# Performance work log

Hardware: AMD Instinct MI355X
Metric: run time of the kernel (lower is better)

The kernel has to match this reference:

```python
import jax, jax.numpy as jnp
import numpy as np

HIDDEN_DIM = 2048
NUM_HEADS = 16
HEAD_DIM = HIDDEN_DIM // NUM_HEADS
BATCH = 2
SEQ = 2048


def setup_inputs() -> dict:
    key = jax.random.key(0)
    ks = jax.random.split(key, 5)
    scale = 1.0 / np.sqrt(HIDDEN_DIM)
    x = jax.random.normal(ks[0], (BATCH, SEQ, HIDDEN_DIM), dtype=jnp.float32)
    w_q = jax.random.normal(ks[1], (HIDDEN_DIM, HIDDEN_DIM), dtype=jnp.float32) * scale
    w_k = jax.random.normal(ks[2], (HIDDEN_DIM, HIDDEN_DIM), dtype=jnp.float32) * scale
    w_v = jax.random.normal(ks[3], (HIDDEN_DIM, HIDDEN_DIM), dtype=jnp.float32) * scale
    w_o = jax.random.normal(ks[4], (HIDDEN_DIM, HIDDEN_DIM), dtype=jnp.float32) * scale
    return {"x": x, "w_q": w_q, "w_k": w_k, "w_v": w_v, "w_o": w_o}


def reference(x, w_q, w_k, w_v, w_o):
    # Projections: x @ W.T  (weights stored as (out, in) like torch)
    q = jnp.einsum('bsd,ed->bse', x, w_q)
    k = jnp.einsum('bsd,ed->bse', x, w_k)
    v = jnp.einsum('bsd,ed->bse', x, w_v)
    b, s, _ = q.shape
    # split heads: (b, h, s, hd)
    q = q.reshape(b, s, NUM_HEADS, HEAD_DIM).transpose(0, 2, 1, 3)
    k = k.reshape(b, s, NUM_HEADS, HEAD_DIM).transpose(0, 2, 1, 3)
    v = v.reshape(b, s, NUM_HEADS, HEAD_DIM).transpose(0, 2, 1, 3)
    scale = 1.0 / np.sqrt(HEAD_DIM)
    # Online-softmax tiling in the source (causal=False default) is
    # mathematically identical to standard softmax attention.
    scores = jnp.einsum('bhqd,bhkd->bhqk', q, k) * scale
    p = jax.nn.softmax(scores, axis=-1)
    o = jnp.einsum('bhqk,bhkd->bhqd', p, v)
    o = o.transpose(0, 2, 1, 3).reshape(b, s, HIDDEN_DIM)
    return jnp.einsum('bsd,ed->bse', o, w_o)
```

## Files before the change

### kernel.cpp

```cpp
#include <hip/hip_runtime.h>


typedef _Float16 half8 __attribute__((ext_vector_type(8)));
typedef _Float16 half4 __attribute__((ext_vector_type(4)));
typedef float floatx4 __attribute__((ext_vector_type(4)));

__device__ __forceinline__ void async16(const void* g, void* l) {
  __builtin_amdgcn_global_load_lds((__attribute__((address_space(1))) void*)(g),
                                   (__attribute__((address_space(3))) void*)(l),
                                   16, 0, 0);
}

__global__ void cvt_all(const float* __restrict__ x, const float* __restrict__ w0,
                        const float* __restrict__ w1, const float* __restrict__ w2,
                        const float* __restrict__ w3, _Float16* __restrict__ xh,
                        _Float16* __restrict__ wh, float scale0) {
  int i = blockIdx.x * blockDim.x + threadIdx.x;
  const int XQ = 1 << 21;
  float sc = 1.0f;
  const float* src;
  _Float16* dst;
  int j;
  if (i < XQ) { src = x; dst = xh; j = i; }
  else {
    int t = i - XQ;
    int m = t >> 20;
    src = (m == 0) ? w0 : (m == 1) ? w1 : (m == 2) ? w2 : w3;
    if (m == 0) sc = scale0;
    dst = wh; j = t;
  }
  int js = (i < XQ) ? j : (j & ((1 << 20) - 1));
  float4 v = reinterpret_cast<const float4*>(src)[js];
  union { _Float16 h[4]; short4 s; } u;
  u.h[0] = (_Float16)(v.x * sc); u.h[1] = (_Float16)(v.y * sc);
  u.h[2] = (_Float16)(v.z * sc); u.h[3] = (_Float16)(v.w * sc);
  reinterpret_cast<short4*>(dst)[j] = u.s;
}

template <int OUT_MODE>
__global__ __launch_bounds__(256)
void gemm_nt(const _Float16* __restrict__ A, const _Float16* __restrict__ Bw,
             void* __restrict__ Cv, void* __restrict__ Cv2) {
  __shared__ _Float16 As[128 * 64];
  __shared__ _Float16 Bs[128 * 64];
  const int tid = threadIdx.x;
  const int wave = tid >> 6, lane = tid & 63;
  const int wm = wave >> 1, wn = wave & 1;
  const int l15 = lane & 15, l4 = lane >> 4;
  const int bm = blockIdx.y, bn = blockIdx.x;

  floatx4 acc[4][4] = {};

  for (int k0 = 0; k0 < 2048; k0 += 64) {
    __syncthreads();
#pragma unroll
    for (int i = 0; i < 4; ++i) {
      int c = i * 256 + tid;
      int row = c >> 3, cc = c & 7;
      int g = cc ^ (row & 7);
      async16(A + (size_t)(bm * 128 + row) * 2048 + k0 + g * 8, &As[c * 8]);
      async16(Bw + (size_t)(bn * 128 + row) * 2048 + k0 + g * 8, &Bs[c * 8]);
    }
    __syncthreads();
#pragma unroll
    for (int ks = 0; ks < 2; ++ks) {
      half8 af[4], bf[4];
      int ch = (ks * 4 + l4) ^ (l15 & 7);
#pragma unroll
      for (int t = 0; t < 4; ++t) {
        af[t] = *reinterpret_cast<const half8*>(&As[(wm * 64 + t * 16 + l15) * 64 + ch * 8]);
        bf[t] = *reinterpret_cast<const half8*>(&Bs[(wn * 64 + t * 16 + l15) * 64 + ch * 8]);
      }
#pragma unroll
      for (int mt = 0; mt < 4; ++mt)
#pragma unroll
        for (int nt = 0; nt < 4; ++nt)
          acc[mt][nt] = __builtin_amdgcn_mfma_f32_16x16x32_f16(af[mt], bf[nt], acc[mt][nt], 0, 0, 0);
    }
  }

  const int rbase = bm * 128 + wm * 64;
  const int cbase = bn * 128 + wn * 64;
  if constexpr (OUT_MODE == 0) {
    if (cbase < 4096) {
      _Float16* C = (_Float16*)Cv + (size_t)(cbase >> 11) * (4096ull * 2048);
#pragma unroll
      for (int mt = 0; mt < 4; ++mt)
#pragma unroll
        for (int nt = 0; nt < 4; ++nt) {
          int r0 = rbase + mt * 16 + l4 * 4;
          int cg = (cbase + nt * 16 + l15) & 2047;
#pragma unroll
          for (int r = 0; r < 4; ++r)
            C[(size_t)(r0 + r) * 2048 + cg] = (_Float16)acc[mt][nt][r];
        }
    } else {
      _Float16* C = (_Float16*)Cv2;
#pragma unroll
      for (int mt = 0; mt < 4; ++mt)
#pragma unroll
        for (int nt = 0; nt < 4; ++nt) {
          int m0 = rbase + mt * 16 + l4 * 4;
          int d = cbase + nt * 16 + l15 - 4096;
          size_t base = (size_t)(m0 >> 11) * (2048ull * 2048) + (size_t)d * 2048 + (m0 & 2047);
          union { _Float16 h[4]; short4 s; } u;
#pragma unroll
          for (int r = 0; r < 4; ++r) u.h[r] = (_Float16)acc[mt][nt][r];
          *reinterpret_cast<short4*>(C + base) = u.s;
        }
    }
  } else {
    float* C = (float*)Cv;
#pragma unroll
    for (int mt = 0; mt < 4; ++mt)
#pragma unroll
      for (int nt = 0; nt < 4; ++nt) {
        int r0 = rbase + mt * 16 + l4 * 4;
        int cg = cbase + nt * 16 + l15;
#pragma unroll
        for (int r = 0; r < 4; ++r)
          C[(size_t)(r0 + r) * 2048 + cg] = acc[mt][nt][r];
      }
  }
}

__global__ __launch_bounds__(256, 2)
void flash_attn(const _Float16* __restrict__ Q, const _Float16* __restrict__ Kg,
                const _Float16* __restrict__ Vt, _Float16* __restrict__ O) {
  __shared__ _Float16 Ks[64 * 128];
  __shared__ _Float16 Vs[128 * 64];
  __shared__ _Float16 Ps[128 * 64];
  const int tid = threadIdx.x, wave = tid >> 6, lane = tid & 63;
  const int l15 = lane & 15, l4 = lane >> 4;
  const int bh = blockIdx.y, b = bh >> 4, h = bh & 15;
  const int q0 = blockIdx.x * 128;

  const _Float16* Qp = Q + ((size_t)(b * 2048 + q0 + wave * 32)) * 2048 + h * 128;
  const _Float16* Kp = Kg + (size_t)b * 2048 * 2048 + h * 128;
  const _Float16* Vp = Vt + (size_t)b * 2048 * 2048 + (size_t)(h * 128) * 2048;

  half8 qf[2][4];
#pragma unroll
  for (int qt = 0; qt < 2; ++qt)
#pragma unroll
    for (int ks = 0; ks < 4; ++ks)
      qf[qt][ks] = *reinterpret_cast<const half8*>(
          Qp + (size_t)(qt * 16 + l15) * 2048 + ks * 32 + l4 * 8);

  floatx4 oacc[2][8] = {};
  float lsumq[2] = {0.f, 0.f};

  for (int k0 = 0; k0 < 2048; k0 += 64) {
    __syncthreads();
#pragma unroll
    for (int i = 0; i < 4; ++i) {
      int c = i * 256 + tid;
      int row = c >> 4, cc = c & 15;
      int g = cc ^ (row & 15);
      async16(Kp + (size_t)(k0 + row) * 2048 + g * 8, &Ks[c * 8]);
    }
#pragma unroll
    for (int i = 0; i < 4; ++i) {
      int c = i * 256 + tid;
      int row = c >> 3, cc = c & 7;
      int g = cc ^ (row & 7);
      async16(Vp + (size_t)row * 2048 + k0 + g * 8, &Vs[c * 8]);
    }
    __syncthreads();

    floatx4 sacc[4][2] = {};
#pragma unroll
    for (int ks = 0; ks < 4; ++ks) {
      half8 kf[4];
#pragma unroll
      for (int st = 0; st < 4; ++st) {
        int row = st * 16 + l15;
        int ch = (ks * 4 + l4) ^ l15;
        kf[st] = *reinterpret_cast<const half8*>(&Ks[row * 128 + ch * 8]);
      }
#pragma unroll
      for (int st = 0; st < 4; ++st)
#pragma unroll
        for (int qt = 0; qt < 2; ++qt)
          sacc[st][qt] = __builtin_amdgcn_mfma_f32_16x16x32_f16(kf[st], qf[qt][ks], sacc[st][qt], 0, 0, 0);
    }

#pragma unroll
    for (int qt = 0; qt < 2; ++qt)
#pragma unroll
      for (int st = 0; st < 4; ++st) {
        float p0 = exp2f(sacc[st][qt][0]);
        float p1 = exp2f(sacc[st][qt][1]);
        float p2 = exp2f(sacc[st][qt][2]);
        float p3 = exp2f(sacc[st][qt][3]);
        lsumq[qt] += (p0 + p1) + (p2 + p3);
        half4 pv;
        pv[0] = (_Float16)p0; pv[1] = (_Float16)p1;
        pv[2] = (_Float16)p2; pv[3] = (_Float16)p3;
        int ch = (st * 2 + (l4 >> 1)) ^ (l15 & 7);
        *reinterpret_cast<half4*>(
            &Ps[(wave * 32 + qt * 16 + l15) * 64 + ch * 8 + (l4 & 1) * 4]) = pv;
      }

    __builtin_amdgcn_s_waitcnt(0xC07F);

#pragma unroll
    for (int ks2 = 0; ks2 < 2; ++ks2) {
      half8 pf[2];
#pragma unroll
      for (int mt = 0; mt < 2; ++mt)
        pf[mt] = *reinterpret_cast<const half8*>(
            &Ps[(wave * 32 + mt * 16 + l15) * 64 + (((ks2 * 4 + l4) ^ (l15 & 7)) * 8)]);
#pragma unroll
      for (int nt2 = 0; nt2 < 8; ++nt2) {
        int row = nt2 * 16 + l15;
        int ch = (ks2 * 4 + l4) ^ (row & 7);
        half8 vf = *reinterpret_cast<const half8*>(&Vs[row * 64 + ch * 8]);
#pragma unroll
        for (int mt = 0; mt < 2; ++mt)
          oacc[mt][nt2] = __builtin_amdgcn_mfma_f32_16x16x32_f16(pf[mt], vf, oacc[mt][nt2], 0, 0, 0);
      }
    }
  }

#pragma unroll
  for (int qt = 0; qt < 2; ++qt) {
    lsumq[qt] += __shfl_xor(lsumq[qt], 16);
    lsumq[qt] += __shfl_xor(lsumq[qt], 32);
  }

  _Float16* Op = O + ((size_t)(b * 2048 + q0 + wave * 32)) * 2048 + h * 128;
#pragma unroll
  for (int mt = 0; mt < 2; ++mt)
#pragma unroll
    for (int r = 0; r < 4; ++r) {
      float inv = 1.0f / __shfl(lsumq[mt], l4 * 4 + r);
#pragma unroll
      for (int nt2 = 0; nt2 < 8; ++nt2) {
        int row = mt * 16 + l4 * 4 + r;
        int col = nt2 * 16 + l15;
        Op[(size_t)row * 2048 + col] = (_Float16)(oacc[mt][nt2][r] * inv);
      }
    }
}

extern "C" void kernel_launch(void* const* d_in, const int* in_sizes, int n_in,
                              void* d_out, int out_size, void* d_ws, size_t ws_size,
                              hipStream_t stream) {
  const float* x = (const float*)d_in[0];
  const float* wq = (const float*)d_in[1];
  const float* wk = (const float*)d_in[2];
  const float* wv = (const float*)d_in[3];
  const float* wo = (const float*)d_in[4];
  float* out = (float*)d_out;

  const size_t XN = (size_t)4096 * 2048;
  const size_t WN = (size_t)2048 * 2048;
  _Float16* xh = (_Float16*)d_ws;
  _Float16* qh = xh + XN;
  _Float16* vth = xh + 3 * XN;
  _Float16* oh = xh + 4 * XN;
  _Float16* wqh = xh + 5 * XN;

  const float SM_SCALE = 0.08838834764831845f * 1.4426950408889634f;

  cvt_all<<<dim3(24576), 256, 0, stream>>>(x, wq, wk, wv, wo, xh, wqh, SM_SCALE);
  gemm_nt<0><<<dim3(48, 32), 256, 0, stream>>>(xh, wqh, qh, vth);
  flash_attn<<<dim3(16, 32), 256, 0, stream>>>(qh, qh + XN, vth, oh);
  gemm_nt<2><<<dim3(16, 32), 256, 0, stream>>>(oh, wqh + 3 * WN, out, nullptr);
}
```

Measured before the change: 392.2 us.

## Rewrite GEMM as 256x128 double-buffered ping-pong pipeline with 512 threads

Restructures the projection GEMM kernel to use 256x128 tiles with 8 waves, double-buffered LDS, and an interleaved schedule that issues async global-to-LDS loads between MFMA clusters guarded by fine-grained vmcnt waits and barriers. Adds s_setprio around MFMA groups and a swizzled block-to-tile mapping for L2 locality. Intended to hide global load latency behind compute and raise MFMA utilization, at the cost of more LDS per block and fragile manual waitcnt ordering.

```diff
diff --git a/kernel.cpp b/kernel.cpp
--- a/kernel.cpp
+++ b/kernel.cpp
@@ -37,59 +37,134 @@
   reinterpret_cast<short4*>(dst)[j] = u.s;
 }
 
+template <int MO, int NO>
+__device__ __forceinline__ void mmg(floatx4 (&acc)[4][4], const half8 (&af)[2][2],
+                                    const half8 (&bf)[2][2]) {
+#pragma unroll
+  for (int mt = 0; mt < 2; ++mt)
+#pragma unroll
+    for (int nt = 0; nt < 2; ++nt)
+#pragma unroll
+      for (int ks = 0; ks < 2; ++ks)
+        acc[MO + mt][NO + nt] = __builtin_amdgcn_mfma_f32_16x16x32_f16(
+            af[mt][ks], bf[nt][ks], acc[MO + mt][NO + nt], 0, 0, 0);
+}
+
+__device__ __forceinline__ void rdfrag(half8 (&f)[2][2], const _Float16* base,
+                                       int r0, int r1, int ch0, int ch1) {
+  f[0][0] = *reinterpret_cast<const half8*>(base + r0 * 64 + ch0);
+  f[0][1] = *reinterpret_cast<const half8*>(base + r0 * 64 + ch1);
+  f[1][0] = *reinterpret_cast<const half8*>(base + r1 * 64 + ch0);
+  f[1][1] = *reinterpret_cast<const half8*>(base + r1 * 64 + ch1);
+}
+
 template <int OUT_MODE>
-__global__ __launch_bounds__(256)
+__global__ __launch_bounds__(512, 2)
 void gemm_nt(const _Float16* __restrict__ A, const _Float16* __restrict__ Bw,
              void* __restrict__ Cv, void* __restrict__ Cv2) {
-  __shared__ _Float16 As[128 * 64];
-  __shared__ _Float16 Bs[128 * 64];
+  __shared__ _Float16 As[2][256 * 64];
+  __shared__ _Float16 Bs[2][128 * 64];
   const int tid = threadIdx.x;
   const int wave = tid >> 6, lane = tid & 63;
   const int wm = wave >> 1, wn = wave & 1;
   const int l15 = lane & 15, l4 = lane >> 4;
-  const int bm = blockIdx.y, bn = blockIdx.x;
+
+  const int nwg = gridDim.x << 4;
+  const int orig = blockIdx.x * 16 + blockIdx.y;
+  const int swz = (orig & 7) * (nwg >> 3) + (orig >> 3);
+  const int bm = swz & 15, bn = swz >> 4;
+
+  const _Float16* ag[4]; int al[4];
+#pragma unroll
+  for (int j = 0; j < 4; ++j) {
+    int c = j * 512 + tid, row = c >> 3, g = (c & 7) ^ (row & 7);
+    ag[j] = A + (size_t)(bm * 256 + row) * 2048 + g * 8;
+    al[j] = c * 8;
+  }
+  const _Float16* bg[2]; int bl[2];
+#pragma unroll
+  for (int j = 0; j < 2; ++j) {
+    int c = j * 512 + tid, row = c >> 3, g = (c & 7) ^ (row & 7);
+    bg[j] = Bw + (size_t)(bn * 128 + row) * 2048 + g * 8;
+    bl[j] = c * 8;
+  }
+
+  const int rm = wm * 16 + l15;
+  const int rn = wn * 16 + l15;
+  const int ch0 = (l4 ^ (l15 & 7)) * 8;
+  const int ch1 = ((l4 + 4) ^ (l15 & 7)) * 8;
+
+#pragma unroll
+  for (int j = 0; j < 4; ++j) async16(ag[j], &As[0][al[j]]);
+#pragma unroll
+  for (int j = 0; j < 2; ++j) async16(bg[j], &Bs[0][bl[j]]);
+  asm volatile("s_waitcnt vmcnt(0)" ::: "memory");
+  __builtin_amdgcn_s_barrier();
 
   floatx4 acc[4][4] = {};
-
-  for (int k0 = 0; k0 < 2048; k0 += 64) {
-    __syncthreads();
-#pragma unroll
-    for (int i = 0; i < 4; ++i) {
-      int c = i * 256 + tid;
-      int row = c >> 3, cc = c & 7;
-      int g = cc ^ (row & 7);
-      async16(A + (size_t)(bm * 128 + row) * 2048 + k0 + g * 8, &As[c * 8]);
-      async16(Bw + (size_t)(bn * 128 + row) * 2048 + k0 + g * 8, &Bs[c * 8]);
-    }
-    __syncthreads();
-#pragma unroll
-    for (int ks = 0; ks < 2; ++ks) {
-      half8 af[4], bf[4];
-      int ch = (ks * 4 + l4) ^ (l15 & 7);
-#pragma unroll
-      for (int t = 0; t < 4; ++t) {
-        af[t] = *reinterpret_cast<const half8*>(&As[(wm * 64 + t * 16 + l15) * 64 + ch * 8]);
-        bf[t] = *reinterpret_cast<const half8*>(&Bs[(wn * 64 + t * 16 + l15) * 64 + ch * 8]);
-      }
+  half8 afA[2][2], afB[2][2], bfA[2][2], bfB[2][2];
+
+#pragma unroll 2
+  for (int t = 0; t < 32; ++t) {
+    const _Float16* Ac = &As[t & 1][0];
+    const _Float16* Bc = &Bs[t & 1][0];
+    _Float16* An = &As[(t & 1) ^ 1][0];
+    _Float16* Bn = &Bs[(t & 1) ^ 1][0];
+    const int kn = t * 64 + 64;
+    const bool st = (t < 31);
+
+    asm volatile("s_waitcnt vmcnt(3)" ::: "memory");
+    rdfrag(afA, Ac, rm, rm + 64, ch0, ch1);
+    if (st) { async16(ag[0] + kn, An + al[0]); async16(ag[1] + kn, An + al[1]); }
+    __builtin_amdgcn_s_barrier();
+    __builtin_amdgcn_s_waitcnt(0xC07F);
+    __builtin_amdgcn_s_setprio(1);
+    if (t) mmg<2, 2>(acc, afB, bfB);
+    __builtin_amdgcn_s_setprio(0);
+    __builtin_amdgcn_s_barrier();
+
+    asm volatile("s_waitcnt vmcnt(4)" ::: "memory");
+    rdfrag(bfA, Bc, rn, rn + 32, ch0, ch1);
+    if (st) async16(bg[0] + kn, Bn + bl[0]);
+    __builtin_amdgcn_s_barrier();
+    __builtin_amdgcn_s_waitcnt(0xC07F);
+    __builtin_amdgcn_s_setprio(1);
+    mmg<0, 0>(acc, afA, bfA);
+    __builtin_amdgcn_s_setprio(0);
+    __builtin_amdgcn_s_barrier();
+
+    asm volatile("s_waitcnt vmcnt(3)" ::: "memory");
+    rdfrag(bfB, Bc, rn + 64, rn + 96, ch0, ch1);
+    if (st) async16(bg[1] + kn, Bn + bl[1]);
+    __builtin_amdgcn_s_barrier();
+    __builtin_amdgcn_s_waitcnt(0xC07F);
+    __builtin_amdgcn_s_setprio(1);
+    mmg<0, 2>(acc, afA, bfB);
+    __builtin_amdgcn_s_setprio(0);
+    __builtin_amdgcn_s_barrier();
+
+    asm volatile("s_waitcnt vmcnt(2)" ::: "memory");
+    rdfrag(afB, Ac, rm + 128, rm + 192, ch0, ch1);
+    if (st) { async16(ag[2] + kn, An + al[2]); async16(ag[3] + kn, An + al[3]); }
+    __builtin_amdgcn_s_barrier();
+    __builtin_amdgcn_s_waitcnt(0xC07F);
+    __builtin_amdgcn_s_setprio(1);
+    mmg<2, 0>(acc, afB, bfA);
+    __builtin_amdgcn_s_setprio(0);
+    __builtin_amdgcn_s_barrier();
+  }
+  mmg<2, 2>(acc, afB, bfB);
+
+  const int cb = bn * 128;
+  if constexpr (OUT_MODE == 0) {
+    if (cb < 4096) {
+      _Float16* C = (_Float16*)Cv + (size_t)(cb >> 11) * (4096ull * 2048);
 #pragma unroll
       for (int mt = 0; mt < 4; ++mt)
 #pragma unroll
-        for (int nt = 0; nt < 4; ++nt)
-          acc[mt][nt] = __builtin_amdgcn_mfma_f32_16x16x32_f16(af[mt], bf[nt], acc[mt][nt], 0, 0, 0);
-    }
-  }
-
-  const int rbase = bm * 128 + wm * 64;
-  const int cbase = bn * 128 + wn * 64;
-  if constexpr (OUT_MODE == 0) {
-    if (cbase < 4096) {
-      _Float16* C = (_Float16*)Cv + (size_t)(cbase >> 11) * (4096ull * 2048);
-#pragma unroll
-      for (int mt = 0; mt < 4; ++mt)
-#pragma unroll
         for (int nt = 0; nt < 4; ++nt) {
-          int r0 = rbase + mt * 16 + l4 * 4;
-          int cg = (cbase + nt * 16 + l15) & 2047;
+          int r0 = bm * 256 + mt * 64 + wm * 16 + l4 * 4;
+          int cg = (cb + nt * 32 + wn * 16 + l15) & 2047;
 #pragma unroll
           for (int r = 0; r < 4; ++r)
             C[(size_t)(r0 + r) * 2048 + cg] = (_Float16)acc[mt][nt][r];
@@ -100,8 +175,8 @@
       for (int mt = 0; mt < 4; ++mt)
 #pragma unroll
         for (int nt = 0; nt < 4; ++nt) {
-          int m0 = rbase + mt * 16 + l4 * 4;
-          int d = cbase + nt * 16 + l15 - 4096;
+          int m0 = bm * 256 + mt * 64 + wm * 16 + l4 * 4;
+          int d = cb + nt * 32 + wn * 16 + l15 - 4096;
           size_t base = (size_t)(m0 >> 11) * (2048ull * 2048) + (size_t)d * 2048 + (m0 & 2047);
           union { _Float16 h[4]; short4 s; } u;
 #pragma unroll
@@ -115,8 +190,8 @@
     for (int mt = 0; mt < 4; ++mt)
 #pragma unroll
       for (int nt = 0; nt < 4; ++nt) {
-        int r0 = rbase + mt * 16 + l4 * 4;
-        int cg = cbase + nt * 16 + l15;
+        int r0 = bm * 256 + mt * 64 + wm * 16 + l4 * 4;
+        int cg = cb + nt * 32 + wn * 16 + l15;
 #pragma unroll
         for (int r = 0; r < 4; ++r)
           C[(size_t)(r0 + r) * 2048 + cg] = acc[mt][nt][r];
@@ -265,7 +340,7 @@
   const float SM_SCALE = 0.08838834764831845f * 1.4426950408889634f;
 
   cvt_all<<<dim3(24576), 256, 0, stream>>>(x, wq, wk, wv, wo, xh, wqh, SM_SCALE);
-  gemm_nt<0><<<dim3(48, 32), 256, 0, stream>>>(xh, wqh, qh, vth);
+  gemm_nt<0><<<dim3(48, 16), 512, 0, stream>>>(xh, wqh, qh, vth);
   flash_attn<<<dim3(16, 32), 256, 0, stream>>>(qh, qh + XN, vth, oh);
-  gemm_nt<2><<<dim3(16, 32), 256, 0, stream>>>(oh, wqh + 3 * WN, out, nullptr);
-}
+  gemm_nt<2><<<dim3(16, 16), 512, 0, stream>>>(oh, wqh + 3 * WN, out, nullptr);
+}
```

After: 409.1 us. +4.3%, slower.

## Rewrite QKV projection GEMM as 256x256 double-buffered pipelined kernel

Applied to the files above, without the earlier changes.

Replaces the fused QKV projection GEMM with a 512-thread, 256x256-tile kernel. It double-buffers LDS, splits each k-step into four MFMA phases interleaved with async global-to-LDS loads and register-level fragment prefetch, and raises wave priority around MFMA bursts. It also swizzles the workgroup order for L2 locality. The aim is to hide load latency and raise MFMA utilisation in the largest GEMM, at the cost of 128KB of LDS, heavy register pressure and hand-tuned waitcnt counts that must stay correct. The output projection moves to a separate copy of the old kernel.

```diff
diff --git a/kernel.cpp b/kernel.cpp
--- a/kernel.cpp
+++ b/kernel.cpp
@@ -37,10 +37,180 @@
   reinterpret_cast<short4*>(dst)[j] = u.s;
 }
 
-template <int OUT_MODE>
-__global__ __launch_bounds__(256)
+__device__ __forceinline__ void rdA4(half8 (&f)[4][2], const _Float16* base,
+                                     int ch0, int ch1) {
+#pragma unroll
+  for (int mt = 0; mt < 4; ++mt) {
+    f[mt][0] = *reinterpret_cast<const half8*>(base + mt * 2048 + ch0);
+    f[mt][1] = *reinterpret_cast<const half8*>(base + mt * 2048 + ch1);
+  }
+}
+__device__ __forceinline__ void rdB2(half8 (&f)[2][2], const _Float16* base,
+                                     int ch0, int ch1) {
+#pragma unroll
+  for (int nt = 0; nt < 2; ++nt) {
+    f[nt][0] = *reinterpret_cast<const half8*>(base + nt * 4096 + ch0);
+    f[nt][1] = *reinterpret_cast<const half8*>(base + nt * 4096 + ch1);
+  }
+}
+template <int MO, int NO>
+__device__ __forceinline__ void mmg16(floatx4 (&acc)[8][4], const half8 (&af)[4][2],
+                                      const half8 (&bf)[2][2]) {
+#pragma unroll
+  for (int kk = 0; kk < 2; ++kk)
+#pragma unroll
+    for (int mt = 0; mt < 4; ++mt)
+#pragma unroll
+      for (int nt = 0; nt < 2; ++nt)
+        acc[MO + mt][NO + nt] = __builtin_amdgcn_mfma_f32_16x16x32_f16(
+            af[mt][kk], bf[nt][kk], acc[MO + mt][NO + nt], 0, 0, 0);
+}
+
+#define STAGE_AH0(buf, kk) { async16(ags + (kk), &(buf)[ldst]); \
+                             async16(ags + 131072 + (kk), &(buf)[4096 + ldst]); }
+#define STAGE_AH1(buf, kk) { async16(ags + 262144 + (kk), &(buf)[8192 + ldst]); \
+                             async16(ags + 393216 + (kk), &(buf)[12288 + ldst]); }
+#define STAGE_BH0(buf, kk) { async16(bgs + (kk), &(buf)[ldst]); \
+                             async16(bgs + 131072 + (kk), &(buf)[4096 + ldst]); }
+#define STAGE_BH1(buf, kk) { async16(bgs + 262144 + (kk), &(buf)[8192 + ldst]); \
+                             async16(bgs + 393216 + (kk), &(buf)[12288 + ldst]); }
+#define VMW(n) asm volatile("s_waitcnt vmcnt(" #n ")" ::: "memory")
+#define SBAR() __builtin_amdgcn_s_barrier()
+#define SCHED() __builtin_amdgcn_sched_barrier(0)
+#define PRIO1() __builtin_amdgcn_s_setprio(1)
+#define PRIO0() __builtin_amdgcn_s_setprio(0)
+
+__global__ __launch_bounds__(512, 2)
 void gemm_nt(const _Float16* __restrict__ A, const _Float16* __restrict__ Bw,
              void* __restrict__ Cv, void* __restrict__ Cv2) {
+  __shared__ _Float16 As[2][256 * 64];
+  __shared__ _Float16 Bs[2][256 * 64];
+  const int tid = threadIdx.x;
+  const int wave = tid >> 6, lane = tid & 63;
+  const int wm = wave >> 2, wn = wave & 3;
+  const int l15 = lane & 15, l4 = lane >> 4;
+
+  const int NBN = 24;
+  const int nwg = NBN * 16;
+  const int swz = (blockIdx.x & 7) * (nwg >> 3) + (blockIdx.x >> 3);
+  const int bn = swz % NBN, bm = swz / NBN;
+
+  const int srow = tid >> 3;
+  const int g = (tid & 7) ^ (srow & 7);
+  const _Float16* ags = A + (size_t)(bm * 256 + srow) * 2048 + g * 8;
+  const _Float16* bgs = Bw + (size_t)(bn * 256 + srow) * 2048 + g * 8;
+  const int ldst = tid * 8;
+
+  const int arow = wm * 16 + l15;
+  const int brow = wn * 16 + l15;
+  const int ch0 = (l4 ^ (l15 & 7)) * 8;
+  const int ch1 = ((l4 + 4) ^ (l15 & 7)) * 8;
+
+  STAGE_AH0(As[0], 0); STAGE_BH0(Bs[0], 0);
+  STAGE_BH1(Bs[0], 0); STAGE_AH1(As[0], 0);
+  STAGE_AH0(As[1], 64); STAGE_BH0(Bs[1], 64);
+  VMW(4);
+  SBAR();
+
+  floatx4 acc[8][4] = {};
+  half8 afA[4][2], afB[4][2], bfA[2][2], bfB[2][2];
+  rdA4(afA, &As[0][arow * 64], ch0, ch1);
+  rdB2(bfA, &Bs[0][brow * 64], ch0, ch1);
+
+#pragma unroll 2
+  for (int t = 0; t < 30; ++t) {
+    const int c = t & 1, nx = c ^ 1;
+    const int k1 = t * 64 + 64, k2 = t * 64 + 128;
+    const _Float16* Ac = &As[c][0];
+    const _Float16* Bc = &Bs[c][0];
+
+    PRIO1(); mmg16<0, 0>(acc, afA, bfA); PRIO0();
+    rdB2(bfB, Bc + brow * 64 + 8192, ch0, ch1);
+    STAGE_BH1(Bs[nx], k1);
+    SCHED(); VMW(6); SBAR();
+
+    PRIO1(); mmg16<0, 2>(acc, afA, bfB); PRIO0();
+    rdA4(afB, Ac + arow * 64 + 8192, ch0, ch1);
+    STAGE_AH1(As[nx], k1);
+    SCHED(); VMW(6); SBAR();
+
+    PRIO1(); mmg16<4, 0>(acc, afB, bfA); PRIO0();
+    STAGE_AH0(As[c], k2);
+    SCHED(); VMW(6); SBAR();
+
+    PRIO1(); mmg16<4, 2>(acc, afB, bfB); PRIO0();
+    rdA4(afA, &As[nx][arow * 64], ch0, ch1);
+    rdB2(bfA, &Bs[nx][brow * 64], ch0, ch1);
+    STAGE_BH0(Bs[c], k2);
+    SCHED(); VMW(6); SBAR();
+  }
+
+  {
+    const _Float16* Ac = &As[0][0];
+    const _Float16* Bc = &Bs[0][0];
+    PRIO1(); mmg16<0, 0>(acc, afA, bfA); PRIO0();
+    rdB2(bfB, Bc + brow * 64 + 8192, ch0, ch1);
+    STAGE_BH1(Bs[1], 1984);
+    SCHED(); VMW(6); SBAR();
+
+    PRIO1(); mmg16<0, 2>(acc, afA, bfB); PRIO0();
+    rdA4(afB, Ac + arow * 64 + 8192, ch0, ch1);
+    STAGE_AH1(As[1], 1984);
+    SCHED(); VMW(6); SBAR();
+
+    PRIO1(); mmg16<4, 0>(acc, afB, bfA); PRIO0();
+    SCHED(); VMW(4); SBAR();
+
+    PRIO1(); mmg16<4, 2>(acc, afB, bfB); PRIO0();
+    rdA4(afA, &As[1][arow * 64], ch0, ch1);
+    rdB2(bfA, &Bs[1][brow * 64], ch0, ch1);
+    SCHED(); VMW(2); SBAR();
+  }
+  {
+    const _Float16* Ac = &As[1][0];
+    const _Float16* Bc = &Bs[1][0];
+    PRIO1(); mmg16<0, 0>(acc, afA, bfA); PRIO0();
+    rdB2(bfB, Bc + brow * 64 + 8192, ch0, ch1);
+    SCHED(); VMW(0); SBAR();
+    PRIO1(); mmg16<0, 2>(acc, afA, bfB); PRIO0();
+    rdA4(afB, Ac + arow * 64 + 8192, ch0, ch1);
+    mmg16<4, 0>(acc, afB, bfA);
+    mmg16<4, 2>(acc, afB, bfB);
+  }
+
+  const int cb0 = bn * 256;
+  if (cb0 < 4096) {
+    _Float16* C = (_Float16*)Cv + (size_t)(cb0 >> 11) * (4096ull * 2048);
+#pragma unroll
+    for (int mt = 0; mt < 8; ++mt)
+#pragma unroll
+      for (int nt = 0; nt < 4; ++nt) {
+        int r0 = bm * 256 + mt * 32 + wm * 16 + l4 * 4;
+        int cg = (cb0 + nt * 64 + wn * 16 + l15) & 2047;
+#pragma unroll
+        for (int r = 0; r < 4; ++r)
+          C[(size_t)(r0 + r) * 2048 + cg] = (_Float16)acc[mt][nt][r];
+      }
+  } else {
+    _Float16* C = (_Float16*)Cv2;
+#pragma unroll
+    for (int mt = 0; mt < 8; ++mt)
+#pragma unroll
+      for (int nt = 0; nt < 4; ++nt) {
+        int m0 = bm * 256 + mt * 32 + wm * 16 + l4 * 4;
+        int d = cb0 + nt * 64 + wn * 16 + l15 - 4096;
+        size_t base = (size_t)(m0 >> 11) * (2048ull * 2048) + (size_t)d * 2048 + (m0 & 2047);
+        union { _Float16 h[4]; short4 s; } u;
+#pragma unroll
+        for (int r = 0; r < 4; ++r) u.h[r] = (_Float16)acc[mt][nt][r];
+        *reinterpret_cast<short4*>(C + base) = u.s;
+      }
+  }
+}
+
+__global__ __launch_bounds__(256)
+void gemm_wo(const _Float16* __restrict__ A, const _Float16* __restrict__ Bw,
+             float* __restrict__ C) {
   __shared__ _Float16 As[128 * 64];
   __shared__ _Float16 Bs[128 * 64];
   const int tid = threadIdx.x;
@@ -57,9 +227,9 @@
     for (int i = 0; i < 4; ++i) {
       int c = i * 256 + tid;
       int row = c >> 3, cc = c & 7;
-      int g = cc ^ (row & 7);
-      async16(A + (size_t)(bm * 128 + row) * 2048 + k0 + g * 8, &As[c * 8]);
-      async16(Bw + (size_t)(bn * 128 + row) * 2048 + k0 + g * 8, &Bs[c * 8]);
+      int gg = cc ^ (row & 7);
+      async16(A + (size_t)(bm * 128 + row) * 2048 + k0 + gg * 8, &As[c * 8]);
+      async16(Bw + (size_t)(bn * 128 + row) * 2048 + k0 + gg * 8, &Bs[c * 8]);
     }
     __syncthreads();
 #pragma unroll
@@ -81,47 +251,16 @@
 
   const int rbase = bm * 128 + wm * 64;
   const int cbase = bn * 128 + wn * 64;
-  if constexpr (OUT_MODE == 0) {
-    if (cbase < 4096) {
-      _Float16* C = (_Float16*)Cv + (size_t)(cbase >> 11) * (4096ull * 2048);
-#pragma unroll
-      for (int mt = 0; mt < 4; ++mt)
-#pragma unroll
-        for (int nt = 0; nt < 4; ++nt) {
-          int r0 = rbase + mt * 16 + l4 * 4;
-          int cg = (cbase + nt * 16 + l15) & 2047;
-#pragma unroll
-          for (int r = 0; r < 4; ++r)
-            C[(size_t)(r0 + r) * 2048 + cg] = (_Float16)acc[mt][nt][r];
-        }
-    } else {
-      _Float16* C = (_Float16*)Cv2;
-#pragma unroll
-      for (int mt = 0; mt < 4; ++mt)
-#pragma unroll
-        for (int nt = 0; nt < 4; ++nt) {
-          int m0 = rbase + mt * 16 + l4 * 4;
-          int d = cbase + nt * 16 + l15 - 4096;
-          size_t base = (size_t)(m0 >> 11) * (2048ull * 2048) + (size_t)d * 2048 + (m0 & 2047);
-          union { _Float16 h[4]; short4 s; } u;
-#pragma unroll
-          for (int r = 0; r < 4; ++r) u.h[r] = (_Float16)acc[mt][nt][r];
-          *reinterpret_cast<short4*>(C + base) = u.s;
-        }
-    }
-  } else {
-    float* C = (float*)Cv;
-#pragma unroll
-    for (int mt = 0; mt < 4; ++mt)
-#pragma unroll
-      for (int nt = 0; nt < 4; ++nt) {
-        int r0 = rbase + mt * 16 + l4 * 4;
-        int cg = cbase + nt * 16 + l15;
-#pragma unroll
-        for (int r = 0; r < 4; ++r)
-          C[(size_t)(r0 + r) * 2048 + cg] = acc[mt][nt][r];
-      }
-  }
+#pragma unroll
+  for (int mt = 0; mt < 4; ++mt)
+#pragma unroll
+    for (int nt = 0; nt < 4; ++nt) {
+      int r0 = rbase + mt * 16 + l4 * 4;
+      int cg = cbase + nt * 16 + l15;
+#pragma unroll
+      for (int r = 0; r < 4; ++r)
+        C[(size_t)(r0 + r) * 2048 + cg] = acc[mt][nt][r];
+    }
 }
 
 __global__ __launch_bounds__(256, 2)
@@ -265,7 +404,7 @@
   const float SM_SCALE = 0.08838834764831845f * 1.4426950408889634f;
 
   cvt_all<<<dim3(24576), 256, 0, stream>>>(x, wq, wk, wv, wo, xh, wqh, SM_SCALE);
-  gemm_nt<0><<<dim3(48, 32), 256, 0, stream>>>(xh, wqh, qh, vth);
+  gemm_nt<<<dim3(384), 512, 0, stream>>>(xh, wqh, qh, vth);
   flash_attn<<<dim3(16, 32), 256, 0, stream>>>(qh, qh + XN, vth, oh);
-  gemm_nt<2><<<dim3(16, 32), 256, 0, stream>>>(oh, wqh + 3 * WN, out, nullptr);
-}
+  gemm_wo<<<dim3(16, 32), 256, 0, stream>>>(oh, wqh + 3 * WN, out);
+}
```

Result: no change. 396.0 us (+1.0%).

## Rewrite QKV projection GEMM with double-buffered LDS pipeline and 128x256 tiles

Applied to the files above, without the earlier changes.

Replaces the fused QKV projection GEMM with a new kernel that uses 128x256 tiles with K-step 32, double-buffered LDS, and async global-to-LDS loads interleaved with the MFMA work. It uses explicit waitcnt, barriers, sched_barrier and setprio to overlap loads with compute. It also remaps block indices in groups of 8 for L2 locality and targets two blocks per CU. The output projection keeps the old simple kernel under a new name. The finer-grained scheduling raises register pressure and adds a risk of hazards if the hand-placed waitcnt counts are wrong.

```diff
diff --git a/kernel.cpp b/kernel.cpp
--- a/kernel.cpp
+++ b/kernel.cpp
@@ -37,10 +37,130 @@
   reinterpret_cast<short4*>(dst)[j] = u.s;
 }
 
-template <int OUT_MODE>
-__global__ __launch_bounds__(256)
+__device__ __forceinline__ void rdA(half8 (&f)[4], const _Float16* base) {
+#pragma unroll
+  for (int mt = 0; mt < 4; ++mt)
+    f[mt] = *reinterpret_cast<const half8*>(base + mt * 512);
+}
+__device__ __forceinline__ void rdB(half8 (&f)[4], const _Float16* base) {
+#pragma unroll
+  for (int nt = 0; nt < 4; ++nt)
+    f[nt] = *reinterpret_cast<const half8*>(base + nt * 2048);
+}
+template <int MO>
+__device__ __forceinline__ void mm16(floatx4 (&acc)[8][4], const half8 (&af)[4],
+                                     const half8 (&bf)[4]) {
+#pragma unroll
+  for (int mt = 0; mt < 4; ++mt)
+#pragma unroll
+    for (int nt = 0; nt < 4; ++nt)
+      acc[MO + mt][nt] = __builtin_amdgcn_mfma_f32_16x16x32_f16(
+          af[mt], bf[nt], acc[MO + mt][nt], 0, 0, 0);
+}
+
+#define STAGE_B(buf, kk) { async16(bgs + (kk), &Bs[buf][bdst]); \
+  async16(bgs + 131072 + (kk), &Bs[buf][bdst + 2048]); \
+  async16(bgs + 262144 + (kk), &Bs[buf][bdst + 4096]); \
+  async16(bgs + 393216 + (kk), &Bs[buf][bdst + 6144]); }
+#define STAGE_A(buf, kk) { async16(ags + (kk), &As[buf][adst]); \
+  async16(ags + 131072 + (kk), &As[buf][adst + 2048]); }
+#define VMW(n) asm volatile("s_waitcnt vmcnt(" #n ")" ::: "memory")
+#define SBAR() __builtin_amdgcn_s_barrier()
+#define SCHED() __builtin_amdgcn_sched_barrier(0)
+#define PRIO1() __builtin_amdgcn_s_setprio(1)
+#define PRIO0() __builtin_amdgcn_s_setprio(0)
+
+__global__ __launch_bounds__(256, 2)
 void gemm_nt(const _Float16* __restrict__ A, const _Float16* __restrict__ Bw,
              void* __restrict__ Cv, void* __restrict__ Cv2) {
+  __shared__ _Float16 As[2][128 * 32];
+  __shared__ _Float16 Bs[2][256 * 32];
+  const int tid = threadIdx.x;
+  const int wn = tid >> 6, lane = tid & 63;
+  const int l15 = lane & 15, l4 = lane >> 4;
+
+  const int swz = (blockIdx.x & 7) * 96 + (blockIdx.x >> 3);
+  const int bn = swz % 24, bm = swz / 24;
+
+  const int srow = tid >> 2;
+  const int sg = (tid & 3) ^ ((srow >> 1) & 3);
+  const _Float16* ags = A + (size_t)(bm * 128 + srow) * 2048 + sg * 8;
+  const _Float16* bgs = Bw + (size_t)(bn * 256 + srow) * 2048 + sg * 8;
+  const int adst = tid * 8, bdst = tid * 8;
+
+  const int rch = (l4 ^ ((l15 >> 1) & 3)) * 8;
+  const int abase = l15 * 32 + rch;
+  const int bbase = (wn * 16 + l15) * 32 + rch;
+
+  STAGE_B(0, 0); STAGE_A(0, 0);
+  STAGE_B(1, 32); STAGE_A(1, 32);
+  VMW(6); SBAR();
+
+  floatx4 acc[8][4] = {};
+  half8 afL[4], afH[4], bf[4];
+  rdA(afL, &As[0][abase]);
+  rdB(bf, &Bs[0][bbase]);
+
+#pragma unroll 2
+  for (int t = 0; t < 62; ++t) {
+    const int c = t & 1, nx = c ^ 1;
+    const int kn = t * 32 + 64;
+
+    PRIO1(); mm16<0>(acc, afL, bf); PRIO0();
+    rdA(afH, &As[c][abase + 2048]);
+    STAGE_B(c, kn);
+    SCHED(); VMW(4); SBAR();
+
+    PRIO1(); mm16<4>(acc, afH, bf); PRIO0();
+    rdA(afL, &As[nx][abase]);
+    rdB(bf, &Bs[nx][bbase]);
+    STAGE_A(c, kn);
+    SCHED(); SBAR();
+  }
+  PRIO1(); mm16<0>(acc, afL, bf); PRIO0();
+  rdA(afH, &As[0][abase + 2048]);
+  SCHED(); VMW(0); SBAR();
+  PRIO1(); mm16<4>(acc, afH, bf); PRIO0();
+  rdA(afL, &As[1][abase]);
+  rdB(bf, &Bs[1][bbase]);
+  SBAR();
+  mm16<0>(acc, afL, bf);
+  rdA(afH, &As[1][abase + 2048]);
+  mm16<4>(acc, afH, bf);
+
+  const int cb0 = bn * 256;
+  if (cb0 < 4096) {
+    _Float16* C = (_Float16*)Cv + (size_t)(cb0 >> 11) * (4096ull * 2048);
+#pragma unroll
+    for (int mt = 0; mt < 8; ++mt)
+#pragma unroll
+      for (int nt = 0; nt < 4; ++nt) {
+        int r0 = bm * 128 + mt * 16 + l4 * 4;
+        int cg = (cb0 + nt * 64 + wn * 16 + l15) & 2047;
+#pragma unroll
+        for (int r = 0; r < 4; ++r)
+          C[(size_t)(r0 + r) * 2048 + cg] = (_Float16)acc[mt][nt][r];
+      }
+  } else {
+    _Float16* C = (_Float16*)Cv2;
+#pragma unroll
+    for (int mt = 0; mt < 8; ++mt)
+#pragma unroll
+      for (int nt = 0; nt < 4; ++nt) {
+        int m0 = bm * 128 + mt * 16 + l4 * 4;
+        int d = cb0 + nt * 64 + wn * 16 + l15 - 4096;
+        size_t base = (size_t)(m0 >> 11) * (2048ull * 2048) + (size_t)d * 2048 + (m0 & 2047);
+        union { _Float16 h[4]; short4 s; } u;
+#pragma unroll
+        for (int r = 0; r < 4; ++r) u.h[r] = (_Float16)acc[mt][nt][r];
+        *reinterpret_cast<short4*>(C + base) = u.s;
+      }
+  }
+}
+
+__global__ __launch_bounds__(256)
+void gemm_wo(const _Float16* __restrict__ A, const _Float16* __restrict__ Bw,
+             float* __restrict__ C) {
   __shared__ _Float16 As[128 * 64];
   __shared__ _Float16 Bs[128 * 64];
   const int tid = threadIdx.x;
@@ -57,9 +177,9 @@
     for (int i = 0; i < 4; ++i) {
       int c = i * 256 + tid;
       int row = c >> 3, cc = c & 7;
-      int g = cc ^ (row & 7);
-      async16(A + (size_t)(bm * 128 + row) * 2048 + k0 + g * 8, &As[c * 8]);
-      async16(Bw + (size_t)(bn * 128 + row) * 2048 + k0 + g * 8, &Bs[c * 8]);
+      int gg = cc ^ (row & 7);
+      async16(A + (size_t)(bm * 128 + row) * 2048 + k0 + gg * 8, &As[c * 8]);
+      async16(Bw + (size_t)(bn * 128 + row) * 2048 + k0 + gg * 8, &Bs[c * 8]);
     }
     __syncthreads();
 #pragma unroll
@@ -81,47 +201,16 @@
 
   const int rbase = bm * 128 + wm * 64;
   const int cbase = bn * 128 + wn * 64;
-  if constexpr (OUT_MODE == 0) {
-    if (cbase < 4096) {
-      _Float16* C = (_Float16*)Cv + (size_t)(cbase >> 11) * (4096ull * 2048);
-#pragma unroll
-      for (int mt = 0; mt < 4; ++mt)
-#pragma unroll
-        for (int nt = 0; nt < 4; ++nt) {
-          int r0 = rbase + mt * 16 + l4 * 4;
-          int cg = (cbase + nt * 16 + l15) & 2047;
-#pragma unroll
-          for (int r = 0; r < 4; ++r)
-            C[(size_t)(r0 + r) * 2048 + cg] = (_Float16)acc[mt][nt][r];
-        }
-    } else {
-      _Float16* C = (_Float16*)Cv2;
-#pragma unroll
-      for (int mt = 0; mt < 4; ++mt)
-#pragma unroll
-        for (int nt = 0; nt < 4; ++nt) {
-          int m0 = rbase + mt * 16 + l4 * 4;
-          int d = cbase + nt * 16 + l15 - 4096;
-          size_t base = (size_t)(m0 >> 11) * (2048ull * 2048) + (size_t)d * 2048 + (m0 & 2047);
-          union { _Float16 h[4]; short4 s; } u;
-#pragma unroll
-          for (int r = 0; r < 4; ++r) u.h[r] = (_Float16)acc[mt][nt][r];
-          *reinterpret_cast<short4*>(C + base) = u.s;
-        }
-    }
-  } else {
-    float* C = (float*)Cv;
-#pragma unroll
-    for (int mt = 0; mt < 4; ++mt)
-#pragma unroll
-      for (int nt = 0; nt < 4; ++nt) {
-        int r0 = rbase + mt * 16 + l4 * 4;
-        int cg = cbase + nt * 16 + l15;
-#pragma unroll
-        for (int r = 0; r < 4; ++r)
-          C[(size_t)(r0 + r) * 2048 + cg] = acc[mt][nt][r];
-      }
-  }
+#pragma unroll
+  for (int mt = 0; mt < 4; ++mt)
+#pragma unroll
+    for (int nt = 0; nt < 4; ++nt) {
+      int r0 = rbase + mt * 16 + l4 * 4;
+      int cg = cbase + nt * 16 + l15;
+#pragma unroll
+      for (int r = 0; r < 4; ++r)
+        C[(size_t)(r0 + r) * 2048 + cg] = acc[mt][nt][r];
+    }
 }
 
 __global__ __launch_bounds__(256, 2)
@@ -265,7 +354,7 @@
   const float SM_SCALE = 0.08838834764831845f * 1.4426950408889634f;
 
   cvt_all<<<dim3(24576), 256, 0, stream>>>(x, wq, wk, wv, wo, xh, wqh, SM_SCALE);
-  gemm_nt<0><<<dim3(48, 32), 256, 0, stream>>>(xh, wqh, qh, vth);
+  gemm_nt<<<dim3(768), 256, 0, stream>>>(xh, wqh, qh, vth);
   flash_attn<<<dim3(16, 32), 256, 0, stream>>>(qh, qh + XN, vth, oh);
-  gemm_nt<2><<<dim3(16, 32), 256, 0, stream>>>(oh, wqh + 3 * WN, out, nullptr);
-}
+  gemm_wo<<<dim3(16, 32), 256, 0, stream>>>(oh, wqh + 3 * WN, out);
+}
```

Result: slower. 407.2 us (+3.8%).
